# Kernel optimization log

Hardware: AMD Instinct MI355X
Metric: run time of the kernel (lower is better)

## Reference

```python
import jax, jax.numpy as jnp
import numpy as np

N_NODES = 100000
SEQ = 16          # spiral length
IN_C = 3
NUM_CLASSES = 12


def _xavier(key, shape):
    fan_out, fan_in = shape
    limit = float(np.sqrt(6.0 / (fan_in + fan_out)))
    return jax.random.uniform(key, shape, jnp.float32, -limit, limit)


def setup_inputs() -> dict:
    key = jax.random.key(0)
    ks = jax.random.split(key, 8)
    x = jax.random.normal(ks[0], (N_NODES, IN_C), jnp.float32)
    indices = jax.random.randint(ks[1], (N_NODES, SEQ), 0, N_NODES, jnp.int64)
    return {
        "x": x,
        "indices": indices,
        "fc0_w": _xavier(ks[2], (16, IN_C)),
        "fc0_b": jnp.zeros((16,), jnp.float32),
        "w1": _xavier(ks[3], (32, 16 * SEQ)),
        "b1": jnp.zeros((32,), jnp.float32),
        "w2": _xavier(ks[4], (64, 32 * SEQ)),
        "b2": jnp.zeros((64,), jnp.float32),
        "w3": _xavier(ks[5], (128, 64 * SEQ)),
        "b3": jnp.zeros((128,), jnp.float32),
        "fc1_w": _xavier(ks[6], (256, 128)),
        "fc1_b": jnp.zeros((256,), jnp.float32),
        "fc2_w": _xavier(ks[7], (NUM_CLASSES, 256)),
        "fc2_b": jnp.zeros((NUM_CLASSES,), jnp.float32),
    }


def _spiral_conv(x, indices, w, b):
    # gather spiral neighborhoods: [N, S, C] -> [N, S*C], then linear
    n = indices.shape[0]
    g = x[indices.reshape(-1)].reshape(n, -1)
    return g @ w.T + b


def reference(x, indices, fc0_w, fc0_b, w1, b1, w2, b2, w3, b3,
              fc1_w, fc1_b, fc2_w, fc2_b):
    h = jax.nn.elu(x @ fc0_w.T + fc0_b)                 # [N, 16]
    h = jax.nn.elu(_spiral_conv(h, indices, w1, b1))    # [N, 32]
    h = jax.nn.elu(_spiral_conv(h, indices, w2, b2))    # [N, 64]
    h = jax.nn.elu(_spiral_conv(h, indices, w3, b3))    # [N, 128]
    h = jax.nn.elu(h @ fc1_w.T + fc1_b)                 # [N, 256]
    # dropout is identity in eval mode
    logits = h @ fc2_w.T + fc2_b                        # [N, num_classes]
    return jax.nn.log_softmax(logits, axis=1)
```

## Files before the change

### kernel.cpp

```cpp
#include <hip/hip_runtime.h>
#include <math.h>
#include <utility>


typedef __bf16 bf16x8 __attribute__((ext_vector_type(8)));
typedef float f32x16 __attribute__((ext_vector_type(16)));

template <int V> using ic = std::integral_constant<int, V>;

template <typename F, int... Is>
__device__ __forceinline__ void static_for_impl(F&& f, std::integer_sequence<int, Is...>) {
    (f(ic<Is>{}), ...);
}
template <int N_, typename F>
__device__ __forceinline__ void static_for(F&& f) {
    static_for_impl(static_cast<F&&>(f), std::make_integer_sequence<int, N_>{});
}

template <int N_>
__device__ __forceinline__ void wait_vmcnt() {
    static_assert(N_ <= 63, "vmcnt range");
    __builtin_amdgcn_s_waitcnt((N_ & 0xF) | (0x7 << 4) | (0xF << 8) | ((N_ >> 4) << 14));
}

__device__ __forceinline__ void memfence_sched() { __builtin_amdgcn_sched_barrier(0x000F); }

__device__ __forceinline__ float elu_f(float v) { return v > 0.f ? v : expm1f(v); }

template <int K, int C>
__device__ __forceinline__ void swz_one(const float* __restrict__ src, __bf16* __restrict__ dst, int j)
{
    int col = j / K;
    int k = j & (K - 1);
    int chunk = ((k >> 6) * 8 + ((k & 63) >> 3)) * C + col;
    dst[chunk * 8 + (k & 7)] = (__bf16)src[j];
}

__global__ __launch_bounds__(256) void cvt_swz_kernel(const float* __restrict__ w1,
                                                      const float* __restrict__ w2,
                                                      const float* __restrict__ w3,
                                                      const float* __restrict__ f1,
                                                      const float* __restrict__ f2,
                                                      __bf16* __restrict__ d1,
                                                      __bf16* __restrict__ d2,
                                                      __bf16* __restrict__ d3,
                                                      __bf16* __restrict__ df1,
                                                      __bf16* __restrict__ df2p)
{
    int i = blockIdx.x * 256 + threadIdx.x;
    if (i < 8192)        swz_one<256, 32>(w1, d1, i);
    else if (i < 40960)  swz_one<512, 64>(w2, d2, i - 8192);
    else if (i < 172032) swz_one<1024, 128>(w3, d3, i - 40960);
    else if (i < 204800) swz_one<128, 256>(f1, df1, i - 172032);
    else if (i < 212992) {
        int d = i - 204800;
        int e = d & 7;
        int chunkIdx = d >> 3;
        int col = chunkIdx & 31;
        int q = chunkIdx >> 5;
        int k = (q >> 3) * 64 + (q & 7) * 8 + e;
        df2p[d] = (col < 12) ? (__bf16)f2[col * 256 + k] : (__bf16)0.f;
    }
}

__global__ __launch_bounds__(256) void idxT_kernel(const int* __restrict__ idx,
                                                   int* __restrict__ idxT, int N)
{
    int i = blockIdx.x * 256 + threadIdx.x;
    if (i >= N * 16) return;
    int n = i >> 4, s = i & 15;
    idxT[s * N + n] = idx[i];
}

__global__ __launch_bounds__(256) void fc0_kernel(const float* __restrict__ x,
                                                  const float* __restrict__ w,
                                                  const float* __restrict__ b,
                                                  __bf16* __restrict__ h0, int N)
{
    int n = blockIdx.x * 256 + threadIdx.x;
    if (n >= N) return;
    float x0 = x[n * 3 + 0], x1 = x[n * 3 + 1], x2 = x[n * 3 + 2];
    __bf16 ob[16];
#pragma unroll
    for (int j = 0; j < 16; ++j)
        ob[j] = (__bf16)elu_f(w[j * 3 + 0] * x0 + w[j * 3 + 1] * x1 + w[j * 3 + 2] * x2 + b[j]);
    int4* dst = (int4*)&h0[(size_t)n * 16];
    dst[0] = *(int4*)&ob[0];
    dst[1] = *(int4*)&ob[8];
}

template <int CIN, int S, int COUT_B, int COUT_TOT, int TILE_M, int RW, int CW,
          bool GATHER, int MINW, int NN>
__global__ __launch_bounds__(256, MINW) void mfma_layer(const __bf16* __restrict__ hin,
                                                        const int* __restrict__ idxT,
                                                        const __bf16* __restrict__ Wsw,
                                                        const float* __restrict__ bias,
                                                        __bf16* __restrict__ hout)
{
    constexpr int K = CIN * S;
    constexpr int NSTEP = K / 64;
    static_assert(K % 64 == 0, "K%64");
    constexpr int WM = TILE_M / RW;
    constexpr int WN = COUT_B / CW;
    constexpr int MT = WM / 32;
    constexpr int NT = WN / 32;
    constexpr int IPS = GATHER ? (64 / CIN) : 1;
    constexpr int D = WM / 8;
    constexpr int Bn = NT * 4;
    constexpr int I = GATHER ? D : 0;
    constexpr int NBUFS = 2;
    static_assert(RW * CW == 4, "4 waves");
    static_assert(WM == 32 || WM == 64, "1-2 row subtiles per wave");

    constexpr int AB = 4 * NBUFS * WM * 128;
    constexpr int CB = TILE_M * (COUT_B + 8) * 2;
    constexpr int SH = AB > CB ? AB : CB;
    __shared__ __align__(16) char smem[SH];

    const int tid = threadIdx.x;
    const int lane = tid & 63;
    const int w = tid >> 6;
    const int wr = w / CW;
    const int wc = w % CW;
    const int ml = lane & 31;
    const int kh = lane >> 5;
    const int m0 = blockIdx.x * TILE_M;
    const int col0 = blockIdx.y * COUT_B;
    const int rbase = m0 + wr * WM;

    char* const Aw = smem + w * (NBUFS * WM * 128);

    int ioff[GATHER ? D : 1];
    int koff[GATHER ? D : 1];
    int gmr[GATHER ? 1 : D];
    int coff[GATHER ? 1 : D];
#pragma unroll
    for (int i = 0; i < D; ++i) {
        int r = i * 8 + (lane >> 3);
        int c = (lane & 7) ^ (r & 7);
        int gm = rbase + r; if (gm >= NN) gm = NN - 1;
        if constexpr (GATHER) {
            ioff[i] = ((c * 8) / CIN) * NN + gm;
            koff[i] = (c * 8) & (CIN - 1);
        } else {
            gmr[i] = gm;
            coff[i] = c * 8;
        }
    }

    bf16x8 bfr[2][NT][4];
    int myIdx[GATHER ? 3 : 1][GATHER ? D : 1];

    const __bf16* wlane = Wsw + ((size_t)(col0 + wc * WN + ml) + (size_t)kh * COUT_TOT) * 8;

    auto loadB = [&](auto sc) {
        constexpr int s = decltype(sc)::value;
        if constexpr (s < NSTEP) {
#pragma unroll
            for (int ni = 0; ni < NT; ++ni)
#pragma unroll
                for (int ks = 0; ks < 4; ++ks)
                    bfr[s & 1][ni][ks] = *(const bf16x8*)(wlane
                        + (size_t)(s * 8 + ks * 2) * COUT_TOT * 8 + ni * 32 * 8);
        }
    };
    auto loadIdxS = [&](auto sc) {
        constexpr int s = decltype(sc)::value;
        if constexpr (GATHER && s < NSTEP) {
#pragma unroll
            for (int i = 0; i < D; ++i)
                myIdx[s % 3][i] = idxT[(s * IPS) * NN + ioff[i]];
        }
    };
    auto issueDMA = [&](auto sc) {
        constexpr int s = decltype(sc)::value;
        if constexpr (s < NSTEP) {
            char* base = Aw + (s % NBUFS) * (WM * 128);
#pragma unroll
            for (int i = 0; i < D; ++i) {
                const __bf16* src;
                if constexpr (GATHER)
                    src = hin + (size_t)myIdx[s % 3][i] * CIN + koff[i];
                else
                    src = hin + (size_t)gmr[i] * K + s * 64 + coff[i];
                __builtin_amdgcn_global_load_lds(
                    (const __attribute__((address_space(1))) void*)src,
                    (__attribute__((address_space(3))) void*)(base + i * 1024),
                    16, 0, 0);
            }
        }
    };

    f32x16 acc[MT][NT];
#pragma unroll
    for (int mi = 0; mi < MT; ++mi)
#pragma unroll
        for (int ni = 0; ni < NT; ++ni) { f32x16 z = {}; acc[mi][ni] = z; }

    loadIdxS(ic<0>{});
    loadIdxS(ic<1>{});
    memfence_sched();
    loadB(ic<0>{});
    memfence_sched();
    issueDMA(ic<0>{});
    memfence_sched();
    loadIdxS(ic<2>{});
    memfence_sched();

    static_for<NSTEP>([&](auto sc) {
        constexpr int s = decltype(sc)::value;
        loadB(ic<s + 1>{});
        memfence_sched();
        issueDMA(ic<s + 1>{});
        memfence_sched();
        loadIdxS(ic<s + 3>{});
        memfence_sched();
        constexpr int NW = I * (s + 2 < NSTEP) + (Bn + D) * (s + 1 < NSTEP)
                         + I * (s + 3 < NSTEP);
        wait_vmcnt<NW>();
        memfence_sched();

        const char* base = Aw + (s % NBUFS) * (WM * 128);
        bf16x8 afr[MT][4];
#pragma unroll
        for (int mi = 0; mi < MT; ++mi)
#pragma unroll
            for (int ks = 0; ks < 4; ++ks) {
                int cb = ks * 2 + kh;
                afr[mi][ks] = *(const bf16x8*)(base + ((mi * 32 + ml) * 8 + (cb ^ (ml & 7))) * 16);
            }
#pragma unroll
        for (int ks = 0; ks < 4; ++ks)
#pragma unroll
            for (int mi = 0; mi < MT; ++mi)
#pragma unroll
                for (int ni = 0; ni < NT; ++ni)
                    acc[mi][ni] = __builtin_amdgcn_mfma_f32_32x32x16_bf16(
                        afr[mi][ks], bfr[s & 1][ni][ks], acc[mi][ni], 0, 0, 0);
    });

    __syncthreads();
    __bf16* Cs = (__bf16*)smem;
    constexpr int LDC = COUT_B + 8;
#pragma unroll
    for (int ni = 0; ni < NT; ++ni) {
        const int col = wc * WN + ni * 32 + ml;
        const float bv = bias[col0 + col];
#pragma unroll
        for (int mi = 0; mi < MT; ++mi) {
#pragma unroll
            for (int r = 0; r < 16; ++r) {
                int row = wr * WM + mi * 32 + ((r & 3) + 8 * (r >> 2) + 4 * kh);
                Cs[row * LDC + col] = (__bf16)elu_f(acc[mi][ni][r] + bv);
            }
        }
    }
    __syncthreads();
    constexpr int C8 = COUT_B / 8;
#pragma unroll
    for (int j2 = tid; j2 < TILE_M * C8; j2 += 256) {
        int row = j2 / C8, c8 = j2 % C8;
        int gm = m0 + row;
        if (gm < NN)
            *(int4*)&hout[(size_t)gm * COUT_TOT + col0 + c8 * 8] = *(int4*)&Cs[row * LDC + c8 * 8];
    }
}

__global__ __launch_bounds__(256, 3) void fc12_kernel(const __bf16* __restrict__ h3,
                                                      const __bf16* __restrict__ Wsw,
                                                      const float* __restrict__ bias1,
                                                      const __bf16* __restrict__ W2p,
                                                      const float* __restrict__ bias2,
                                                      float* __restrict__ out)
{
    __shared__ __align__(16) char smem[32 * 264 * 2];
    const int tid = threadIdx.x;
    const int lane = tid & 63;
    const int w = tid >> 6;
    const int ml = lane & 31;
    const int kh = lane >> 5;
    const int m0 = blockIdx.x * 32;

    const __bf16* wlane = Wsw + ((size_t)(w * 64 + ml) + (size_t)kh * 256) * 8;
    bf16x8 bfr[2][2][4];
#pragma unroll
    for (int s = 0; s < 2; ++s)
#pragma unroll
        for (int ni = 0; ni < 2; ++ni)
#pragma unroll
            for (int ks = 0; ks < 4; ++ks)
                bfr[s][ni][ks] = *(const bf16x8*)(wlane
                    + (size_t)(s * 8 + ks * 2) * 256 * 8 + ni * 32 * 8);

    bf16x8 b2f[4];
#pragma unroll
    for (int ks = 0; ks < 4; ++ks)
        b2f[ks] = *(const bf16x8*)&W2p[((w * 8 + ks * 2 + kh) * 32 + ml) * 8];

#pragma unroll
    for (int t = 0; t < 2; ++t) {
        int j = w * 2 + t;
        int lr = j * 4 + (lane >> 4);
        int sc = (lane & 15) ^ (lr & 15);
        const __bf16* src = h3 + (size_t)(m0 + lr) * 128 + sc * 8;
        __builtin_amdgcn_global_load_lds(
            (const __attribute__((address_space(1))) void*)src,
            (__attribute__((address_space(3))) void*)(smem + j * 1024),
            16, 0, 0);
    }
    wait_vmcnt<0>();
    __syncthreads();

    f32x16 acc[2];
    { f32x16 z = {}; acc[0] = z; acc[1] = z; }
    const char* Ab = smem;
#pragma unroll
    for (int s = 0; s < 2; ++s) {
        bf16x8 afr[4];
#pragma unroll
        for (int ks = 0; ks < 4; ++ks) {
            int c16 = s * 8 + ks * 2 + kh;
            afr[ks] = *(const bf16x8*)(Ab + ml * 256 + ((c16 ^ (ml & 15)) * 16));
        }
#pragma unroll
        for (int ks = 0; ks < 4; ++ks)
#pragma unroll
            for (int ni = 0; ni < 2; ++ni)
                acc[ni] = __builtin_amdgcn_mfma_f32_32x32x16_bf16(afr[ks], bfr[s][ni][ks], acc[ni], 0, 0, 0);
    }
    __syncthreads();

    __bf16* Cs = (__bf16*)smem;
#pragma unroll
    for (int ni = 0; ni < 2; ++ni) {
        int col = w * 64 + ni * 32 + ml;
        float bv = bias1[col];
#pragma unroll
        for (int r = 0; r < 16; ++r) {
            int row = (r & 3) + 8 * (r >> 2) + 4 * kh;
            Cs[row * 264 + col] = (__bf16)elu_f(acc[ni][r] + bv);
        }
    }
    __syncthreads();

    bf16x8 a2[4];
#pragma unroll
    for (int ks = 0; ks < 4; ++ks)
        a2[ks] = *(const bf16x8*)&Cs[ml * 264 + w * 64 + ks * 16 + kh * 8];
    f32x16 acc2;
    { f32x16 z = {}; acc2 = z; }
#pragma unroll
    for (int ks = 0; ks < 4; ++ks)
        acc2 = __builtin_amdgcn_mfma_f32_32x32x16_bf16(a2[ks], b2f[ks], acc2, 0, 0, 0);
    __syncthreads();

    float* P = (float*)(smem + w * 4096);
#pragma unroll
    for (int r = 0; r < 16; ++r)
        P[((r & 3) + 8 * (r >> 2) + 4 * kh) * 32 + ml] = acc2[r];
    __syncthreads();

    float4 s4 = make_float4(0.f, 0.f, 0.f, 0.f);
#pragma unroll
    for (int pw = 0; pw < 4; ++pw) {
        float4 v = *(float4*)(smem + pw * 4096 + tid * 16);
        s4.x += v.x; s4.y += v.y; s4.z += v.z; s4.w += v.w;
    }
    __syncthreads();
    *(float4*)(smem + tid * 16) = s4;
    __syncthreads();

    if (tid < 32) {
        const float* L = (float*)smem + tid * 32;
        float logits[12], mx = -1e30f;
#pragma unroll
        for (int o = 0; o < 12; ++o) {
            logits[o] = L[o] + bias2[o];
            mx = fmaxf(mx, logits[o]);
        }
        float s = 0.f;
#pragma unroll
        for (int o = 0; o < 12; ++o) s += expf(logits[o] - mx);
        float lse = mx + logf(s);
        int n = m0 + tid;
        float4 o0 = make_float4(logits[0] - lse, logits[1] - lse, logits[2] - lse, logits[3] - lse);
        float4 o1 = make_float4(logits[4] - lse, logits[5] - lse, logits[6] - lse, logits[7] - lse);
        float4 o2 = make_float4(logits[8] - lse, logits[9] - lse, logits[10] - lse, logits[11] - lse);
        *(float4*)&out[(size_t)n * 12 + 0] = o0;
        *(float4*)&out[(size_t)n * 12 + 4] = o1;
        *(float4*)&out[(size_t)n * 12 + 8] = o2;
    }
}

extern "C" void kernel_launch(void* const* d_in, const int* in_sizes, int n_in,
                              void* d_out, int out_size, void* d_ws, size_t ws_size,
                              hipStream_t stream)
{
    const int N = 100000;
    const float* x     = (const float*)d_in[0];
    const int*   idx   = (const int*)  d_in[1];
    const float* fc0_w = (const float*)d_in[2];
    const float* fc0_b = (const float*)d_in[3];
    const float* w1    = (const float*)d_in[4];
    const float* b1    = (const float*)d_in[5];
    const float* w2    = (const float*)d_in[6];
    const float* b2    = (const float*)d_in[7];
    const float* w3    = (const float*)d_in[8];
    const float* b3    = (const float*)d_in[9];
    const float* fc1_w = (const float*)d_in[10];
    const float* fc1_b = (const float*)d_in[11];
    const float* fc2_w = (const float*)d_in[12];
    const float* fc2_b = (const float*)d_in[13];
    float* out = (float*)d_out;

    char* ws = (char*)d_ws;
    const int n_w1 = 32 * 256, n_w2 = 64 * 512, n_w3 = 128 * 1024, n_fc1 = 256 * 128;
    const int n_fc2p = 32 * 256;
    const int n_wb = n_w1 + n_w2 + n_w3 + n_fc1 + n_fc2p;
    __bf16* w1b = (__bf16*)ws;
    __bf16* w2b = w1b + n_w1;
    __bf16* w3b = w2b + n_w2;
    __bf16* f1b = w3b + n_w3;
    __bf16* f2b = f1b + n_fc1;
    size_t off = ((size_t)n_wb * 2 + 4095) & ~(size_t)4095;
    int* idxT = (int*)(ws + off);      off += (size_t)N * 16 * 4;
    __bf16* h0 = (__bf16*)(ws + off);  off += (size_t)N * 16 * 2;
    __bf16* h1 = (__bf16*)(ws + off);  off += (size_t)N * 32 * 2;
    __bf16* h2 = (__bf16*)(ws + off);  off += (size_t)N * 64 * 2;
    __bf16* h3 = (__bf16*)(ws + off);  off += (size_t)N * 128 * 2;

    cvt_swz_kernel<<<(n_wb + 255) / 256, 256, 0, stream>>>(w1, w2, w3, fc1_w, fc2_w,
                                                           w1b, w2b, w3b, f1b, f2b);
    idxT_kernel<<<(N * 16 + 255) / 256, 256, 0, stream>>>(idx, idxT, N);
    fc0_kernel<<<(N + 255) / 256, 256, 0, stream>>>(x, fc0_w, fc0_b, h0, N);

    mfma_layer<16, 16, 32, 32, 128, 4, 1, true, 3, 100000>
        <<<dim3((N + 127) / 128, 1), 256, 0, stream>>>(h0, idxT, w1b, b1, h1);
    mfma_layer<32, 16, 64, 64, 128, 4, 1, true, 3, 100000>
        <<<dim3((N + 127) / 128, 1), 256, 0, stream>>>(h1, idxT, w2b, b2, h2);
    mfma_layer<64, 16, 128, 128, 64, 2, 2, true, 3, 100000>
        <<<dim3((N + 63) / 64, 1), 256, 0, stream>>>(h2, idxT, w3b, b3, h3);
    fc12_kernel<<<N / 32, 256, 0, stream>>>(h3, f1b, fc1_b, f2b, fc2_b, out);
}
```

Measured before the change: 228.9 us.

## Store layer-2 activations as FP8 and dequantize in the layer-3 gather kernel

Layer 2 now writes its ELU output as FP8 e4m3 instead of bf16, halving the h2 buffer. A new dedicated layer-3 kernel gathers the FP8 rows with global-to-LDS loads and dequantizes them to bf16 in registers before the MFMAs. This is meant to cut the random-gather memory traffic of the largest spiral layer, at the price of lower activation precision and extra per-element conversion work.

```diff
diff --git a/kernel.cpp b/kernel.cpp
--- a/kernel.cpp
+++ b/kernel.cpp
@@ -1,4 +1,5 @@
 #include <hip/hip_runtime.h>
+#include <hip/hip_fp8.h>
 #include <math.h>
 #include <utility>
 
@@ -26,6 +27,22 @@
 __device__ __forceinline__ void memfence_sched() { __builtin_amdgcn_sched_barrier(0x000F); }
 
 __device__ __forceinline__ float elu_f(float v) { return v > 0.f ? v : expm1f(v); }
+
+__device__ __forceinline__ unsigned char to_fp8(float v) {
+    __hip_fp8_e4m3 q(v);
+    return (unsigned char)q.__x;
+}
+
+__device__ __forceinline__ bf16x8 dq8(long v) {
+    bf16x8 r;
+#pragma unroll
+    for (int j = 0; j < 8; ++j) {
+        __hip_fp8_e4m3 q;
+        q.__x = (unsigned char)(v >> (8 * j));
+        r[j] = (__bf16)(float)q;
+    }
+    return r;
+}
 
 template <int K, int C>
 __device__ __forceinline__ void swz_one(const float* __restrict__ src, __bf16* __restrict__ dst, int j)
@@ -90,12 +107,12 @@
 }
 
 template <int CIN, int S, int COUT_B, int COUT_TOT, int TILE_M, int RW, int CW,
-          bool GATHER, int MINW, int NN>
+          bool GATHER, bool OUTF8, int MINW, int NN>
 __global__ __launch_bounds__(256, MINW) void mfma_layer(const __bf16* __restrict__ hin,
                                                         const int* __restrict__ idxT,
                                                         const __bf16* __restrict__ Wsw,
                                                         const float* __restrict__ bias,
-                                                        __bf16* __restrict__ hout)
+                                                        void* __restrict__ hout)
 {
     constexpr int K = CIN * S;
     constexpr int NSTEP = K / 64;
@@ -113,7 +130,7 @@
     static_assert(WM == 32 || WM == 64, "1-2 row subtiles per wave");
 
     constexpr int AB = 4 * NBUFS * WM * 128;
-    constexpr int CB = TILE_M * (COUT_B + 8) * 2;
+    constexpr int CB = OUTF8 ? TILE_M * (COUT_B + 16) : TILE_M * (COUT_B + 8) * 2;
     constexpr int SH = AB > CB ? AB : CB;
     __shared__ __align__(16) char smem[SH];
 
@@ -240,29 +257,194 @@
     });
 
     __syncthreads();
+    if constexpr (OUTF8) {
+        unsigned char* Cs8 = (unsigned char*)smem;
+        constexpr int LDC8 = COUT_B + 16;
+#pragma unroll
+        for (int ni = 0; ni < NT; ++ni) {
+            const int col = wc * WN + ni * 32 + ml;
+            const float bv = bias[col0 + col];
+#pragma unroll
+            for (int mi = 0; mi < MT; ++mi) {
+#pragma unroll
+                for (int r = 0; r < 16; ++r) {
+                    int row = wr * WM + mi * 32 + ((r & 3) + 8 * (r >> 2) + 4 * kh);
+                    Cs8[row * LDC8 + col] = to_fp8(elu_f(acc[mi][ni][r] + bv));
+                }
+            }
+        }
+        __syncthreads();
+        constexpr int C16 = COUT_B / 16;
+#pragma unroll
+        for (int j2 = tid; j2 < TILE_M * C16; j2 += 256) {
+            int row = j2 / C16, c16 = j2 % C16;
+            int gm = m0 + row;
+            if (gm < NN)
+                *(int4*)((unsigned char*)hout + (size_t)gm * COUT_TOT + col0 + c16 * 16)
+                    = *(int4*)&Cs8[row * LDC8 + c16 * 16];
+        }
+    } else {
+        __bf16* Cs = (__bf16*)smem;
+        constexpr int LDC = COUT_B + 8;
+#pragma unroll
+        for (int ni = 0; ni < NT; ++ni) {
+            const int col = wc * WN + ni * 32 + ml;
+            const float bv = bias[col0 + col];
+#pragma unroll
+            for (int mi = 0; mi < MT; ++mi) {
+#pragma unroll
+                for (int r = 0; r < 16; ++r) {
+                    int row = wr * WM + mi * 32 + ((r & 3) + 8 * (r >> 2) + 4 * kh);
+                    Cs[row * LDC + col] = (__bf16)elu_f(acc[mi][ni][r] + bv);
+                }
+            }
+        }
+        __syncthreads();
+        constexpr int C8 = COUT_B / 8;
+#pragma unroll
+        for (int j2 = tid; j2 < TILE_M * C8; j2 += 256) {
+            int row = j2 / C8, c8 = j2 % C8;
+            int gm = m0 + row;
+            if (gm < NN)
+                *(int4*)&((__bf16*)hout)[(size_t)gm * COUT_TOT + col0 + c8 * 8] = *(int4*)&Cs[row * LDC + c8 * 8];
+        }
+    }
+}
+
+__global__ __launch_bounds__(256, 3) void mfma3_mixed(const unsigned char* __restrict__ h2f8,
+                                                      const int* __restrict__ idxT,
+                                                      const __bf16* __restrict__ Wsw,
+                                                      const float* __restrict__ bias,
+                                                      __bf16* __restrict__ h3)
+{
+    constexpr int NN = 100000;
+    constexpr int NSTEP = 16;
+    constexpr int D = 2;
+    constexpr int Bn = 8;
+    constexpr int I = 2;
+    __shared__ __align__(16) char smem[17408];
+
+    const int tid = threadIdx.x;
+    const int lane = tid & 63;
+    const int w = tid >> 6;
+    const int wr = w >> 1;
+    const int wc = w & 1;
+    const int ml = lane & 31;
+    const int kh = lane >> 5;
+    const int m0 = blockIdx.x * 64;
+    const int rbase = m0 + wr * 32;
+
+    char* const Aw = smem + w * 4096;
+
+    int ioff[D], koff[D];
+#pragma unroll
+    for (int i = 0; i < D; ++i) {
+        int r = i * 16 + (lane >> 2);
+        int c = (lane & 3) ^ (r & 3);
+        int gm = rbase + r; if (gm >= NN) gm = NN - 1;
+        ioff[i] = gm;
+        koff[i] = c * 16;
+    }
+
+    bf16x8 bfr[2][2][4];
+    int myIdx[3][D];
+
+    const __bf16* wlane = Wsw + ((size_t)(wc * 64 + ml) + (size_t)kh * 128) * 8;
+
+    auto loadB = [&](auto sc) {
+        constexpr int s = decltype(sc)::value;
+        if constexpr (s < NSTEP) {
+#pragma unroll
+            for (int ni = 0; ni < 2; ++ni)
+#pragma unroll
+                for (int ks = 0; ks < 4; ++ks)
+                    bfr[s & 1][ni][ks] = *(const bf16x8*)(wlane
+                        + (size_t)(s * 8 + ks * 2) * 128 * 8 + ni * 32 * 8);
+        }
+    };
+    auto loadIdxS = [&](auto sc) {
+        constexpr int s = decltype(sc)::value;
+        if constexpr (s < NSTEP) {
+#pragma unroll
+            for (int i = 0; i < D; ++i)
+                myIdx[s % 3][i] = idxT[(size_t)s * NN + ioff[i]];
+        }
+    };
+    auto issueDMA = [&](auto sc) {
+        constexpr int s = decltype(sc)::value;
+        if constexpr (s < NSTEP) {
+            char* base = Aw + (s & 1) * 2048;
+#pragma unroll
+            for (int i = 0; i < D; ++i) {
+                const unsigned char* src = h2f8 + (size_t)myIdx[s % 3][i] * 64 + koff[i];
+                __builtin_amdgcn_global_load_lds(
+                    (const __attribute__((address_space(1))) void*)src,
+                    (__attribute__((address_space(3))) void*)(base + i * 1024),
+                    16, 0, 0);
+            }
+        }
+    };
+
+    f32x16 acc[2];
+    { f32x16 z = {}; acc[0] = z; acc[1] = z; }
+
+    loadIdxS(ic<0>{});
+    loadIdxS(ic<1>{});
+    memfence_sched();
+    loadB(ic<0>{});
+    memfence_sched();
+    issueDMA(ic<0>{});
+    memfence_sched();
+    loadIdxS(ic<2>{});
+    memfence_sched();
+
+    static_for<NSTEP>([&](auto sc) {
+        constexpr int s = decltype(sc)::value;
+        loadB(ic<s + 1>{});
+        memfence_sched();
+        issueDMA(ic<s + 1>{});
+        memfence_sched();
+        loadIdxS(ic<s + 3>{});
+        memfence_sched();
+        constexpr int NW = I * (s + 2 < NSTEP) + (Bn + D) * (s + 1 < NSTEP)
+                         + I * (s + 3 < NSTEP);
+        wait_vmcnt<NW>();
+        memfence_sched();
+
+        const char* base = Aw + (s & 1) * 2048;
+        bf16x8 afr[4];
+#pragma unroll
+        for (int ks = 0; ks < 4; ++ks) {
+            long a8 = *(const long*)(base + ml * 64 + ((ks ^ (ml & 3)) << 4) + kh * 8);
+            afr[ks] = dq8(a8);
+        }
+#pragma unroll
+        for (int ks = 0; ks < 4; ++ks)
+#pragma unroll
+            for (int ni = 0; ni < 2; ++ni)
+                acc[ni] = __builtin_amdgcn_mfma_f32_32x32x16_bf16(
+                    afr[ks], bfr[s & 1][ni][ks], acc[ni], 0, 0, 0);
+    });
+
+    __syncthreads();
     __bf16* Cs = (__bf16*)smem;
-    constexpr int LDC = COUT_B + 8;
-#pragma unroll
-    for (int ni = 0; ni < NT; ++ni) {
-        const int col = wc * WN + ni * 32 + ml;
-        const float bv = bias[col0 + col];
-#pragma unroll
-        for (int mi = 0; mi < MT; ++mi) {
-#pragma unroll
-            for (int r = 0; r < 16; ++r) {
-                int row = wr * WM + mi * 32 + ((r & 3) + 8 * (r >> 2) + 4 * kh);
-                Cs[row * LDC + col] = (__bf16)elu_f(acc[mi][ni][r] + bv);
-            }
-        }
-    }
-    __syncthreads();
-    constexpr int C8 = COUT_B / 8;
-#pragma unroll
-    for (int j2 = tid; j2 < TILE_M * C8; j2 += 256) {
-        int row = j2 / C8, c8 = j2 % C8;
+#pragma unroll
+    for (int ni = 0; ni < 2; ++ni) {
+        const int col = wc * 64 + ni * 32 + ml;
+        const float bv = bias[col];
+#pragma unroll
+        for (int r = 0; r < 16; ++r) {
+            int row = wr * 32 + ((r & 3) + 8 * (r >> 2) + 4 * kh);
+            Cs[row * 136 + col] = (__bf16)elu_f(acc[ni][r] + bv);
+        }
+    }
+    __syncthreads();
+#pragma unroll
+    for (int j2 = tid; j2 < 64 * 16; j2 += 256) {
+        int row = j2 >> 4, c8 = j2 & 15;
         int gm = m0 + row;
         if (gm < NN)
-            *(int4*)&hout[(size_t)gm * COUT_TOT + col0 + c8 * 8] = *(int4*)&Cs[row * LDC + c8 * 8];
+            *(int4*)&h3[(size_t)gm * 128 + c8 * 8] = *(int4*)&Cs[row * 136 + c8 * 8];
     }
 }
 
@@ -423,22 +605,21 @@
     __bf16* f1b = w3b + n_w3;
     __bf16* f2b = f1b + n_fc1;
     size_t off = ((size_t)n_wb * 2 + 4095) & ~(size_t)4095;
-    int* idxT = (int*)(ws + off);      off += (size_t)N * 16 * 4;
-    __bf16* h0 = (__bf16*)(ws + off);  off += (size_t)N * 16 * 2;
-    __bf16* h1 = (__bf16*)(ws + off);  off += (size_t)N * 32 * 2;
-    __bf16* h2 = (__bf16*)(ws + off);  off += (size_t)N * 64 * 2;
-    __bf16* h3 = (__bf16*)(ws + off);  off += (size_t)N * 128 * 2;
+    int* idxT = (int*)(ws + off);              off += (size_t)N * 16 * 4;
+    __bf16* h0 = (__bf16*)(ws + off);          off += (size_t)N * 16 * 2;
+    __bf16* h1 = (__bf16*)(ws + off);          off += (size_t)N * 32 * 2;
+    unsigned char* h2f8 = (unsigned char*)(ws + off);  off += (size_t)N * 64;
+    __bf16* h3 = (__bf16*)(ws + off);          off += (size_t)N * 128 * 2;
 
     cvt_swz_kernel<<<(n_wb + 255) / 256, 256, 0, stream>>>(w1, w2, w3, fc1_w, fc2_w,
                                                            w1b, w2b, w3b, f1b, f2b);
     idxT_kernel<<<(N * 16 + 255) / 256, 256, 0, stream>>>(idx, idxT, N);
     fc0_kernel<<<(N + 255) / 256, 256, 0, stream>>>(x, fc0_w, fc0_b, h0, N);
 
-    mfma_layer<16, 16, 32, 32, 128, 4, 1, true, 3, 100000>
-        <<<dim3((N + 127) / 128, 1), 256, 0, stream>>>(h0, idxT, w1b, b1, h1);
-    mfma_layer<32, 16, 64, 64, 128, 4, 1, true, 3, 100000>
-        <<<dim3((N + 127) / 128, 1), 256, 0, stream>>>(h1, idxT, w2b, b2, h2);
-    mfma_layer<64, 16, 128, 128, 64, 2, 2, true, 3, 100000>
-        <<<dim3((N + 63) / 64, 1), 256, 0, stream>>>(h2, idxT, w3b, b3, h3);
+    mfma_layer<16, 16, 32, 32, 128, 4, 1, true, false, 3, 100000>
+        <<<dim3((N + 127) / 128, 1), 256, 0, stream>>>(h0, idxT, w1b, b1, (void*)h1);
+    mfma_layer<32, 16, 64, 64, 128, 4, 1, true, true, 3, 100000>
+        <<<dim3((N + 127) / 128, 1), 256, 0, stream>>>(h1, idxT, w2b, b2, (void*)h2f8);
+    mfma3_mixed<<<(N + 63) / 64, 256, 0, stream>>>(h2f8, idxT, w3b, b3, h3);
     fc12_kernel<<<N / 32, 256, 0, stream>>>(h3, f1b, fc1_b, f2b, fc2_b, out);
 }
```

New measurement: 226.3 us (median of 2 runs). No clear change (-1.1%).
